# Optimization experiments

Measured on AMD Instinct MI355X. Metric: run time of the kernel, lower is better.

## Reference

```python
import jax, jax.numpy as jnp
import numpy as np

RAW_ID_SPACE = 500_000   # raw id universe (fill_max)
MAX_VOCAB = 1_000_000    # max_vocabulary_size (rows of embedding_var)
EMB_DIM = 128            # embedding_vec_size
IDS_SHAPE = (4096, 26, 8)


def setup_inputs() -> dict:
    key = jax.random.key(0)
    k1, k2 = jax.random.split(key)
    ids = jax.random.randint(k1, IDS_SHAPE, 0, RAW_ID_SPACE, dtype=jnp.int32)
    embedding_var = jax.random.uniform(
        k2, (MAX_VOCAB, EMB_DIM), dtype=jnp.float32, minval=-0.05, maxval=0.05)
    default_embedding = jnp.zeros((1, EMB_DIM), dtype=jnp.float32)
    return {"ids": ids, "embedding_var": embedding_var,
            "default_embedding": default_embedding}


def reference(ids, embedding_var, default_embedding):
    # Training path of HashtableEmbedding.call starting from an empty hash
    # table and counter=0: each raw id is assigned a slot equal to its
    # first-appearance rank in the flattened id stream (tf.unique order),
    # then embeddings are gathered at those slots.
    flat = ids.reshape(-1)                       # [N]
    n = flat.shape[0]
    pos = jnp.arange(n, dtype=jnp.int32)
    # first occurrence position of each raw id (scatter-min over raw space)
    first_pos = jax.ops.segment_min(pos, flat, num_segments=RAW_ID_SPACE)
    fp = first_pos[flat]                         # [N] first pos of my id
    is_first = (fp == pos)
    rank = jnp.cumsum(is_first.astype(jnp.int32)) - 1  # first-appearance rank
    hash_ids = rank[fp]                          # [N] slot in [0, n_unique)
    # table = [embedding_var ; default_embedding]; slot V selects default row
    table = jnp.concatenate([embedding_var, default_embedding], axis=0)
    emb = table[hash_ids]                        # [N, D] irregular gather
    return emb.reshape(ids.shape + (embedding_var.shape[1],))
```

## Files before the change

kernel.cpp:

```cpp
#include <hip/hip_runtime.h>

#define N_IDS   851968
#define RAW     500000
#define EPB     1024
#define NBLK    (N_IDS / EPB)
#define TOTAL_F4 (N_IDS * 32)
#define STREAM_F4 (TOTAL_F4 / 8)

typedef float f32x4 __attribute__((ext_vector_type(4)));

__device__ __forceinline__ int wave_incl_scan(int v) {
    int lane = threadIdx.x & 63;
#pragma unroll
    for (int d = 1; d < 64; d <<= 1) {
        int n = __shfl_up(v, d, 64);
        if (lane >= d) v += n;
    }
    return v;
}

__global__ void k_init(int* __restrict__ first_pos) {
    int i = blockIdx.x * 256 + threadIdx.x;
    if (i < RAW) first_pos[i] = 0x7f7f7f7f;
}

__global__ void k_first_pos(const int* __restrict__ flat, int* __restrict__ first_pos) {
    int i = blockIdx.x * 256 + threadIdx.x;
    atomicMin(&first_pos[flat[i]], i);
}

__global__ void k_block_sums(const int* __restrict__ flat, const int* __restrict__ first_pos,
                             int* __restrict__ bsums) {
    int tid = threadIdx.x;
    int4 f4 = reinterpret_cast<const int4*>(flat)[blockIdx.x * 256 + tid];
    int base = blockIdx.x * EPB + tid * 4;
    int s = 0;
    s += (first_pos[f4.x] == base + 0);
    s += (first_pos[f4.y] == base + 1);
    s += (first_pos[f4.z] == base + 2);
    s += (first_pos[f4.w] == base + 3);
#pragma unroll
    for (int d = 32; d >= 1; d >>= 1) s += __shfl_down(s, d, 64);
    __shared__ int wsum[4];
    int wid = tid >> 6, lane = tid & 63;
    if (lane == 0) wsum[wid] = s;
    __syncthreads();
    if (tid == 0) bsums[blockIdx.x] = wsum[0] + wsum[1] + wsum[2] + wsum[3];
}

__global__ void k_rank_slot(const int* __restrict__ flat, const int* __restrict__ first_pos,
                            const int* __restrict__ bsums, int* __restrict__ slot) {
    int tid = threadIdx.x;
    int wid = tid >> 6, lane = tid & 63;
    __shared__ int wsum[4];
    __shared__ int sboff;

    int partial = 0;
    for (int j = tid; j < blockIdx.x; j += 256) partial += bsums[j];
#pragma unroll
    for (int d = 32; d >= 1; d >>= 1) partial += __shfl_down(partial, d, 64);
    if (lane == 0) wsum[wid] = partial;
    __syncthreads();
    if (tid == 0) sboff = wsum[0] + wsum[1] + wsum[2] + wsum[3];
    __syncthreads();

    int4 f4 = reinterpret_cast<const int4*>(flat)[blockIdx.x * 256 + tid];
    int base = blockIdx.x * EPB + tid * 4;
    int f[4] = {f4.x, f4.y, f4.z, f4.w};
    int flg[4], s = 0;
#pragma unroll
    for (int j = 0; j < 4; ++j) {
        flg[j] = (first_pos[f[j]] == base + j);
        s += flg[j];
    }
    int incl = wave_incl_scan(s);
    if (lane == 63) wsum[wid] = incl;
    __syncthreads();
    int woff = 0;
    for (int w = 0; w < wid; ++w) woff += wsum[w];
    int off = sboff + woff + (incl - s);
#pragma unroll
    for (int j = 0; j < 4; ++j) {
        if (flg[j]) { slot[f[j]] = off; ++off; }
    }
}

__global__ void __launch_bounds__(256) k_gather(
        const int* __restrict__ flat, const int* __restrict__ slot,
        const f32x4* __restrict__ emb, f32x4* __restrict__ out) {
    int t = blockIdx.x * 256 + threadIdx.x;
    int idx[8];
    int r[8];
#pragma unroll
    for (int k = 0; k < 8; ++k) {
        idx[k] = t + k * STREAM_F4;
        r[k] = slot[flat[idx[k] >> 5]];
    }
    f32x4 v[8];
#pragma unroll
    for (int k = 0; k < 8; ++k)
        v[k] = emb[(size_t)r[k] * 32 + (idx[k] & 31)];
#pragma unroll
    for (int k = 0; k < 8; ++k)
        __builtin_nontemporal_store(v[k], &out[idx[k]]);
}

extern "C" void kernel_launch(void* const* d_in, const int* in_sizes, int n_in,
                              void* d_out, int out_size, void* d_ws, size_t ws_size,
                              hipStream_t stream) {
    const int*   ids = (const int*)d_in[0];
    const float* emb = (const float*)d_in[1];

    char* ws = (char*)d_ws;
    int* first_pos = (int*)(ws);
    int* slot      = (int*)(ws + 2000000);
    int* bsums     = (int*)(ws + 4000000);

    k_init      <<<(RAW + 255) / 256, 256, 0, stream>>>(first_pos);
    k_first_pos <<<N_IDS / 256, 256, 0, stream>>>(ids, first_pos);
    k_block_sums<<<NBLK, 256, 0, stream>>>(ids, first_pos, bsums);
    k_rank_slot <<<NBLK, 256, 0, stream>>>(ids, first_pos, bsums, slot);
    k_gather    <<<STREAM_F4 / 256, 256, 0, stream>>>(ids, slot,
                     (const f32x4*)emb, (f32x4*)d_out);
}
```

Baseline: 196.9 us.

## Sort output rows by embedding slot before gathering to improve table locality

Adds a counting sort of output rows keyed by their hash slot: count per slot, prefix-scan into cursors, then atomically scatter row indices into slot order. The gather then walks rows in slot order, so the 128-float embedding reads become nearly sequential and duplicate slots hit in cache, and it uses a block swizzle plus two half-stream loads per thread. The cost is four extra kernels, more atomics and workspace traffic, and output writes that now land scattered rather than streaming.

```diff
diff --git a/kernel.cpp b/kernel.cpp
--- a/kernel.cpp
+++ b/kernel.cpp
@@ -4,8 +4,8 @@
 #define RAW     500000
 #define EPB     1024
 #define NBLK    (N_IDS / EPB)
-#define TOTAL_F4 (N_IDS * 32)
-#define STREAM_F4 (TOTAL_F4 / 8)
+#define CBLK    ((RAW + EPB - 1) / EPB)
+#define HALF_W  (N_IDS / 2)
 
 typedef float f32x4 __attribute__((ext_vector_type(4)));
 
@@ -19,9 +19,9 @@
     return v;
 }
 
-__global__ void k_init(int* __restrict__ first_pos) {
-    int i = blockIdx.x * 256 + threadIdx.x;
-    if (i < RAW) first_pos[i] = 0x7f7f7f7f;
+__global__ void k_init(int* __restrict__ first_pos, int* __restrict__ count) {
+    int i = blockIdx.x * 256 + threadIdx.x;
+    if (i < RAW) { first_pos[i] = 0x7f7f7f7f; count[i] = 0; }
 }
 
 __global__ void k_first_pos(const int* __restrict__ flat, int* __restrict__ first_pos) {
@@ -85,24 +85,91 @@
     }
 }
 
+__global__ void k_row_slot_cnt(const int* __restrict__ flat, const int* __restrict__ slot,
+                               int* __restrict__ rslot, int* __restrict__ count) {
+    int i = blockIdx.x * 256 + threadIdx.x;
+    int rs = slot[flat[i]];
+    rslot[i] = rs;
+    atomicAdd(&count[rs], 1);
+}
+
+__global__ void k_cnt_bsums(const int* __restrict__ count, int* __restrict__ cbs) {
+    int tid = threadIdx.x;
+    int e = blockIdx.x * 256 + tid;
+    int s = 0;
+    if (e < RAW / 4) {
+        int4 c4 = reinterpret_cast<const int4*>(count)[e];
+        s = c4.x + c4.y + c4.z + c4.w;
+    }
+#pragma unroll
+    for (int d = 32; d >= 1; d >>= 1) s += __shfl_down(s, d, 64);
+    __shared__ int wsum[4];
+    int wid = tid >> 6, lane = tid & 63;
+    if (lane == 0) wsum[wid] = s;
+    __syncthreads();
+    if (tid == 0) cbs[blockIdx.x] = wsum[0] + wsum[1] + wsum[2] + wsum[3];
+}
+
+__global__ void k_cursor(const int* __restrict__ count, const int* __restrict__ cbs,
+                         int* __restrict__ cursor) {
+    int tid = threadIdx.x;
+    int wid = tid >> 6, lane = tid & 63;
+    __shared__ int wsum[4];
+    __shared__ int sboff;
+
+    int partial = 0;
+    for (int j = tid; j < blockIdx.x; j += 256) partial += cbs[j];
+#pragma unroll
+    for (int d = 32; d >= 1; d >>= 1) partial += __shfl_down(partial, d, 64);
+    if (lane == 0) wsum[wid] = partial;
+    __syncthreads();
+    if (tid == 0) sboff = wsum[0] + wsum[1] + wsum[2] + wsum[3];
+    __syncthreads();
+
+    int e = blockIdx.x * 256 + tid;
+    int4 c4 = {0, 0, 0, 0};
+    if (e < RAW / 4) c4 = reinterpret_cast<const int4*>(count)[e];
+    int s = c4.x + c4.y + c4.z + c4.w;
+    int incl = wave_incl_scan(s);
+    if (lane == 63) wsum[wid] = incl;
+    __syncthreads();
+    int woff = 0;
+    for (int w = 0; w < wid; ++w) woff += wsum[w];
+    int base = sboff + woff + (incl - s);
+    if (e < RAW / 4) {
+        int q = e * 4;
+        cursor[q + 0] = base;
+        cursor[q + 1] = base + c4.x;
+        cursor[q + 2] = base + c4.x + c4.y;
+        cursor[q + 3] = base + c4.x + c4.y + c4.z;
+    }
+}
+
+__global__ void k_scatter(const int* __restrict__ rslot, int* __restrict__ cursor,
+                          int* __restrict__ order) {
+    int i = blockIdx.x * 256 + threadIdx.x;
+    int rs = rslot[i];
+    int pos = atomicAdd(&cursor[rs], 1);
+    order[pos] = i;
+}
+
 __global__ void __launch_bounds__(256) k_gather(
-        const int* __restrict__ flat, const int* __restrict__ slot,
+        const int* __restrict__ order, const int* __restrict__ rslot,
         const f32x4* __restrict__ emb, f32x4* __restrict__ out) {
-    int t = blockIdx.x * 256 + threadIdx.x;
-    int idx[8];
-    int r[8];
-#pragma unroll
-    for (int k = 0; k < 8; ++k) {
-        idx[k] = t + k * STREAM_F4;
-        r[k] = slot[flat[idx[k] >> 5]];
-    }
-    f32x4 v[8];
-#pragma unroll
-    for (int k = 0; k < 8; ++k)
-        v[k] = emb[(size_t)r[k] * 32 + (idx[k] & 31)];
-#pragma unroll
-    for (int k = 0; k < 8; ++k)
-        __builtin_nontemporal_store(v[k], &out[idx[k]]);
+    int bid = blockIdx.x;
+    int swz = (bid & 7) * (53248 >> 3) + (bid >> 3);
+    int t = swz * 256 + threadIdx.x;
+    int c = t & 31;
+    int w0 = t >> 5;
+    int w1 = w0 + HALF_W;
+    int row0 = order[w0];
+    int row1 = order[w1];
+    int rs0 = rslot[row0];
+    int rs1 = rslot[row1];
+    f32x4 v0 = emb[(size_t)rs0 * 32 + c];
+    f32x4 v1 = emb[(size_t)rs1 * 32 + c];
+    __builtin_nontemporal_store(v0, &out[(size_t)row0 * 32 + c]);
+    __builtin_nontemporal_store(v1, &out[(size_t)row1 * 32 + c]);
 }
 
 extern "C" void kernel_launch(void* const* d_in, const int* in_sizes, int n_in,
@@ -114,12 +181,21 @@
     char* ws = (char*)d_ws;
     int* first_pos = (int*)(ws);
     int* slot      = (int*)(ws + 2000000);
-    int* bsums     = (int*)(ws + 4000000);
-
-    k_init      <<<(RAW + 255) / 256, 256, 0, stream>>>(first_pos);
-    k_first_pos <<<N_IDS / 256, 256, 0, stream>>>(ids, first_pos);
-    k_block_sums<<<NBLK, 256, 0, stream>>>(ids, first_pos, bsums);
-    k_rank_slot <<<NBLK, 256, 0, stream>>>(ids, first_pos, bsums, slot);
-    k_gather    <<<STREAM_F4 / 256, 256, 0, stream>>>(ids, slot,
-                     (const f32x4*)emb, (f32x4*)d_out);
-}
+    int* count     = (int*)(ws + 4000000);
+    int* cursor    = (int*)(ws + 6000000);
+    int* bsums     = (int*)(ws + 8000000);
+    int* cbs       = (int*)(ws + 8003328);
+    int* rslot     = (int*)(ws + 8005376);
+    int* order     = (int*)(ws + 11413248);
+
+    k_init        <<<(RAW + 255) / 256, 256, 0, stream>>>(first_pos, count);
+    k_first_pos   <<<N_IDS / 256, 256, 0, stream>>>(ids, first_pos);
+    k_block_sums  <<<NBLK, 256, 0, stream>>>(ids, first_pos, bsums);
+    k_rank_slot   <<<NBLK, 256, 0, stream>>>(ids, first_pos, bsums, slot);
+    k_row_slot_cnt<<<N_IDS / 256, 256, 0, stream>>>(ids, slot, rslot, count);
+    k_cnt_bsums   <<<CBLK, 256, 0, stream>>>(count, cbs);
+    k_cursor      <<<CBLK, 256, 0, stream>>>(count, cbs, cursor);
+    k_scatter     <<<N_IDS / 256, 256, 0, stream>>>(rslot, cursor, order);
+    k_gather      <<<53248, 256, 0, stream>>>(order, rslot,
+                       (const f32x4*)emb, (f32x4*)d_out);
+}
```

Result: slower. 219.0 us (+11.2%).
